# Kernel optimization log

Measured on AMD Instinct MI355X. Metric: run time of the kernel, lower is better.

## Reference

```python
import math
import jax, jax.numpy as jnp
import numpy as np

B, H, S, D = 2, 16, 2048, 64

def setup_inputs() -> dict:
    key = jax.random.key(0)
    kq, kk, kv = jax.random.split(key, 3)
    return {
        "query": jax.random.normal(kq, (B, H, S, D), dtype=jnp.float32),
        "key": jax.random.normal(kk, (B, H, S, D), dtype=jnp.float32),
        "value": jax.random.normal(kv, (B, H, S, D), dtype=jnp.float32),
        "mask": jnp.ones((B, S, 1), dtype=jnp.float32),  # padding mask, 1 = keep
        "mask_now": 0,  # 0 -> causal (tril diag=0); 1 -> strict causal (diag=-1)
    }

def reference(query, key, value, mask, mask_now):
    d_k = query.shape[-1]
    seq_len = mask.shape[1]
    # [B,H,S,S] scaled scores
    attn_scores = jnp.einsum("bhqd,bhkd->bhqk", query, key) / math.sqrt(d_k)
    diag = -1 if mask_now else 0
    triu_mask = jnp.tril(jnp.ones((seq_len, seq_len), dtype=mask.dtype), diag)  # [S,S]
    # mask[:, :, 0] -> per-query padding mask broadcast over key dim: [B,1,S,S]
    full_mask = triu_mask[None, None, :, :] * mask[:, None, :, 0:1]
    attn_scores = jnp.where(full_mask == 0, jnp.float32(-1e9), attn_scores)
    attn_scores = jax.nn.softmax(attn_scores, axis=-1)
    output = jnp.einsum("bhqk,bhkd->bhqd", attn_scores, value)
    return (output, attn_scores)
```

## Files before the change

### kernel.cpp

```cpp
#include <hip/hip_runtime.h>
#include <math.h>

#define NB 2
#define NH 16
#define SL 2048
#define DD 64
#define KC 64
#define NCH (SL / KC)
#define NT 256
#define LPS 68

typedef short bf16x8 __attribute__((ext_vector_type(8)));
typedef float f32x4  __attribute__((ext_vector_type(4)));

__device__ __forceinline__ unsigned short f2bf(float x) {
    unsigned u = __float_as_uint(x);
    u += 0x7fffu + ((u >> 16) & 1u);
    return (unsigned short)(u >> 16);
}

__device__ __forceinline__ void lds_barrier() {
    asm volatile("s_waitcnt lgkmcnt(0)\n\ts_barrier" ::: "memory");
}

__global__ __launch_bounds__(256)
void cvt_bf16(const float* __restrict__ in, unsigned short* __restrict__ out,
              int n4, float scale)
{
    int i = blockIdx.x * 256 + threadIdx.x;
    if (i >= n4) return;
    float4 v = ((const float4*)in)[i];
    ushort4 o;
    o.x = f2bf(v.x * scale); o.y = f2bf(v.y * scale);
    o.z = f2bf(v.z * scale); o.w = f2bf(v.w * scale);
    ((ushort4*)out)[i] = o;
}

__global__ __launch_bounds__(256)
void transpose_v(const float* __restrict__ V, unsigned short* __restrict__ Vt)
{
    __shared__ __align__(16) unsigned short vt[64 * 72];
    const int bh = blockIdx.x >> 5;
    const int s0 = (blockIdx.x & 31) * 64;
    const int t  = threadIdx.x;

    const float4* src = (const float4*)(V + ((size_t)bh * SL + s0) * DD);
    #pragma unroll
    for (int i = 0; i < 4; ++i) {
        int idx = t + i * 256;
        int r = idx >> 4, d4 = idx & 15;
        float4 v = src[r * 16 + d4];
        vt[(d4 * 4 + 0) * 72 + r] = f2bf(v.x);
        vt[(d4 * 4 + 1) * 72 + r] = f2bf(v.y);
        vt[(d4 * 4 + 2) * 72 + r] = f2bf(v.z);
        vt[(d4 * 4 + 3) * 72 + r] = f2bf(v.w);
    }
    __syncthreads();
    const int d = t >> 2, seg = t & 3;
    unsigned short* dst = Vt + ((size_t)bh * DD + d) * SL + s0 + seg * 16;
    uint4 p0 = *(const uint4*)&vt[d * 72 + seg * 16];
    uint4 p1 = *(const uint4*)&vt[d * 72 + seg * 16 + 8];
    *(uint4*)dst = p0;
    *(uint4*)(dst + 8) = p1;
}

__global__ __launch_bounds__(NT, 4)
void attn_mfma(const unsigned short* __restrict__ Qb,
               const unsigned short* __restrict__ Kb,
               const unsigned short* __restrict__ Vt,
               const float* __restrict__ Mg,
               const int* __restrict__ MNg,
               float* __restrict__ Og)
{
    __shared__ __align__(16) float ps[4][16 * LPS];
    __shared__ float lsx[4][16];

    const int tid  = threadIdx.x;
    const int w    = tid >> 6;
    const int lane = tid & 63;
    const int l15  = lane & 15;
    const int qd   = lane >> 4;

    const int lin  = blockIdx.x;
    const int xcd  = lin & 7;
    const int iloc = lin >> 3;
    const int bh   = xcd * 4 + (iloc >> 6);
    const int g    = iloc & 63;
    const int j    = (iloc >> 5) & 7;
    const int b    = bh >> 4;

    const int role  = (w + j) & 3;
    const int khalf = role & 1;
    const int r0    = (role < 2) ? g * 16 : 2032 - g * 16;

    const int diag = (MNg[0] != 0) ? -1 : 0;

    int rlim[4]; int anyDeg = 0;
    #pragma unroll
    for (int reg = 0; reg < 4; ++reg) {
        int row = r0 + qd * 4 + reg;
        float m = Mg[(size_t)b * SL + row];
        int rl = row + diag;
        if (m == 0.0f) rl = -1;
        rlim[reg] = rl;
        anyDeg |= (rl < 0);
    }
    const bool grpDeg = __any(anyDeg);
    const int lastB = grpDeg ? (NCH - 1) : ((r0 + 15 + diag) >> 6);
    const int N     = lastB + 1;
    const int kcMid = N >> 1;
    const int kcBeg = khalf ? kcMid : 0;
    const int kcEnd = khalf ? N : kcMid;

    const unsigned short* Qh  = Qb + (size_t)bh * SL * DD;
    const unsigned short* Kh  = Kb + (size_t)bh * SL * DD;
    const unsigned short* Vth = Vt + (size_t)bh * DD * SL;
    float* Oo   = Og + ((size_t)bh * SL + r0) * DD;
    float* Sout = Og + (size_t)NB * NH * SL * DD
                     + (size_t)bh * SL * SL + (size_t)r0 * SL;
    float* slab = ps[role];

    const unsigned short* qrow = Qh + (size_t)(r0 + l15) * DD + qd * 8;
    bf16x8 qf0 = *(const bf16x8*)qrow;
    bf16x8 qf1 = *(const bf16x8*)(qrow + 32);

    auto ldK = [&](int it, bf16x8& f0, bf16x8& f1) {
        const unsigned short* kr = Kh + (size_t)(it * 16 + l15) * DD + qd * 8;
        f0 = *(const bf16x8*)kr;
        f1 = *(const bf16x8*)(kr + 32);
    };

    float lacc[4] = {0.0f, 0.0f, 0.0f, 0.0f};
    {
        const int t0 = kcBeg * 4;
        const int T  = (kcEnd - kcBeg) * 4;
        auto cmpA = [&](int it, bf16x8 f0, bf16x8 f1) {
            f32x4 acc = {0.0f, 0.0f, 0.0f, 0.0f};
            __builtin_amdgcn_s_setprio(1);
            acc = __builtin_amdgcn_mfma_f32_16x16x32_bf16(qf0, f0, acc, 0, 0, 0);
            acc = __builtin_amdgcn_mfma_f32_16x16x32_bf16(qf1, f1, acc, 0, 0, 0);
            __builtin_amdgcn_s_setprio(0);
            const int col = it * 16 + l15;
            #pragma unroll
            for (int reg = 0; reg < 4; ++reg)
                lacc[reg] += (col <= rlim[reg]) ? __builtin_exp2f(acc[reg]) : 0.0f;
        };
        if (T > 0) {
            bf16x8 A0, A1, B0, B1;
            ldK(t0, A0, A1);
            for (int t = 0; t < T; t += 2) {
                if (t + 1 < T) ldK(t0 + t + 1, B0, B1);
                cmpA(t0 + t, A0, A1);
                if (t + 2 < T) ldK(t0 + t + 2, A0, A1);
                if (t + 1 < T) cmpA(t0 + t + 1, B0, B1);
            }
        }
    }

    float lsum[4];
    #pragma unroll
    for (int reg = 0; reg < 4; ++reg) {
        float s = lacc[reg];
        s += __shfl_xor(s, 1);  s += __shfl_xor(s, 2);
        s += __shfl_xor(s, 4);  s += __shfl_xor(s, 8);
        lsum[reg] = s;
    }
    if (l15 == 0) {
        #pragma unroll
        for (int reg = 0; reg < 4; ++reg)
            lsx[role][qd * 4 + reg] = lsum[reg];
    }
    lds_barrier();
    float pmul[4], pfill[4];
    #pragma unroll
    for (int reg = 0; reg < 4; ++reg) {
        float tot = lsum[reg] + lsx[role ^ 1][qd * 4 + reg];
        pmul[reg]  = (rlim[reg] < 0) ? 0.0f : 1.0f / tot;
        pfill[reg] = (rlim[reg] < 0) ? (1.0f / (float)SL) : 0.0f;
    }

    f32x4 oacc[4];
    #pragma unroll
    for (int nt = 0; nt < 4; ++nt) oacc[nt] = (f32x4){0.0f, 0.0f, 0.0f, 0.0f};

    for (int kc = kcBeg; kc < kcEnd; ++kc) {
        const int c0 = kc * KC;
        bf16x8 kb0[2], kb1[2];
        ldK(kc * 4, kb0[0], kb1[0]);
        #pragma unroll
        for (int nt = 0; nt < 4; ++nt) {
            if (nt < 3) ldK(kc * 4 + nt + 1, kb0[(nt + 1) & 1], kb1[(nt + 1) & 1]);
            f32x4 acc = {0.0f, 0.0f, 0.0f, 0.0f};
            __builtin_amdgcn_s_setprio(1);
            acc = __builtin_amdgcn_mfma_f32_16x16x32_bf16(qf0, kb0[nt & 1], acc, 0, 0, 0);
            acc = __builtin_amdgcn_mfma_f32_16x16x32_bf16(qf1, kb1[nt & 1], acc, 0, 0, 0);
            __builtin_amdgcn_s_setprio(0);
            const int col = c0 + nt * 16 + l15;
            #pragma unroll
            for (int reg = 0; reg < 4; ++reg) {
                float val = (col <= rlim[reg]) ? __builtin_exp2f(acc[reg]) * pmul[reg]
                                               : pfill[reg];
                slab[(qd * 4 + reg) * LPS + nt * 16 + l15] = val;
            }
        }
        bf16x8 vb0[2], vb1[2];
        {
            const unsigned short* vr = Vth + (size_t)l15 * SL + c0 + qd * 8;
            vb0[0] = *(const bf16x8*)vr;
            vb1[0] = *(const bf16x8*)(vr + 32);
        }
        #pragma unroll
        for (int ii = 0; ii < 4; ++ii) {
            int idx = ii * 64 + lane;
            int rr = idx >> 4, c4 = idx & 15;
            *(float4*)(Sout + (size_t)rr * SL + c0 + c4 * 4) =
                *(const float4*)&slab[rr * LPS + c4 * 4];
        }
        bf16x8 paf[2];
        #pragma unroll
        for (int kb = 0; kb < 2; ++kb) {
            const float* pr = &slab[l15 * LPS + kb * 32 + qd * 8];
            float4 x = *(const float4*)pr;
            float4 y = *(const float4*)(pr + 4);
            bf16x8 f;
            f[0] = (short)f2bf(x.x); f[1] = (short)f2bf(x.y);
            f[2] = (short)f2bf(x.z); f[3] = (short)f2bf(x.w);
            f[4] = (short)f2bf(y.x); f[5] = (short)f2bf(y.y);
            f[6] = (short)f2bf(y.z); f[7] = (short)f2bf(y.w);
            paf[kb] = f;
        }
        #pragma unroll
        for (int nt = 0; nt < 4; ++nt) {
            if (nt < 3) {
                const unsigned short* vr = Vth + (size_t)((nt + 1) * 16 + l15) * SL + c0 + qd * 8;
                vb0[(nt + 1) & 1] = *(const bf16x8*)vr;
                vb1[(nt + 1) & 1] = *(const bf16x8*)(vr + 32);
            }
            __builtin_amdgcn_s_setprio(1);
            oacc[nt] = __builtin_amdgcn_mfma_f32_16x16x32_bf16(paf[0], vb0[nt & 1], oacc[nt], 0, 0, 0);
            oacc[nt] = __builtin_amdgcn_mfma_f32_16x16x32_bf16(paf[1], vb1[nt & 1], oacc[nt], 0, 0, 0);
            __builtin_amdgcn_s_setprio(0);
        }
    }

    {
        const int zMid = N + ((NCH - N) >> 1);
        const int zb = khalf ? zMid : N;
        const int ze = khalf ? NCH : zMid;
        float4 z = make_float4(0.0f, 0.0f, 0.0f, 0.0f);
        for (int kc = zb; kc < ze; ++kc) {
            const int c0 = kc * KC;
            #pragma unroll
            for (int ii = 0; ii < 4; ++ii) {
                int idx = ii * 64 + lane;
                int rr = idx >> 4, c4 = idx & 15;
                *(float4*)(Sout + (size_t)rr * SL + c0 + c4 * 4) = z;
            }
        }
    }

    #pragma unroll
    for (int nt = 0; nt < 4; ++nt)
        #pragma unroll
        for (int reg = 0; reg < 4; ++reg)
            slab[(qd * 4 + reg) * LPS + nt * 16 + l15] = oacc[nt][reg];
    lds_barrier();
    {
        const float* sA = ps[role & ~1];
        const float* sB = ps[role | 1];
        #pragma unroll
        for (int ii = 0; ii < 2; ++ii) {
            int idx = ii * 64 + lane;
            int rr = (idx >> 4) + khalf * 8;
            int c4 = idx & 15;
            float4 a = *(const float4*)&sA[rr * LPS + c4 * 4];
            float4 bv = *(const float4*)&sB[rr * LPS + c4 * 4];
            float4 o = make_float4(a.x + bv.x, a.y + bv.y, a.z + bv.z, a.w + bv.w);
            *(float4*)(Oo + (size_t)rr * DD + c4 * 4) = o;
        }
    }
}

extern "C" void kernel_launch(void* const* d_in, const int* in_sizes, int n_in,
                              void* d_out, int out_size, void* d_ws, size_t ws_size,
                              hipStream_t stream)
{
    const float* q  = (const float*)d_in[0];
    const float* k  = (const float*)d_in[1];
    const float* v  = (const float*)d_in[2];
    const float* mk = (const float*)d_in[3];
    const int*   mn = (const int*)d_in[4];
    float* out = (float*)d_out;

    const size_t nElem = (size_t)NB * NH * SL * DD;
    unsigned short* Qb = (unsigned short*)d_ws;
    unsigned short* Kp = Qb + nElem;
    unsigned short* Vp = Kp + nElem;

    const int n4 = (int)(nElem / 4);
    cvt_bf16<<<n4 / 256, 256, 0, stream>>>(q, Qb, n4, 0.125f * 1.44269504f);
    cvt_bf16<<<n4 / 256, 256, 0, stream>>>(k, Kp, n4, 1.0f);
    transpose_v<<<NB * NH * (SL / 64), 256, 0, stream>>>(v, Vp);

    attn_mfma<<<2048, NT, 0, stream>>>(Qb, Kp, Vp, mk, mn, out);
}
```

Baseline: 744.5 us.

## Raise occupancy target and drop software-pipelined K/V register prefetch

Raises the launch-bounds minimum blocks per CU from 4 to 8, which forces the compiler to use fewer registers. To fit that budget it removes the double-buffered K and V fragment prefetching in the normalization pass and the main loop, loading each fragment right before its MFMA. It also rewrites the zero-fill of masked score columns so each half-wave fills 8 full rows contiguously instead of splitting chunks. The intent is to hide latency through more resident waves rather than explicit prefetch, at the risk of exposed load latency per wave and possible register spills.

```diff
diff --git a/kernel.cpp b/kernel.cpp
--- a/kernel.cpp
+++ b/kernel.cpp
@@ -64,7 +64,7 @@
     *(uint4*)(dst + 8) = p1;
 }
 
-__global__ __launch_bounds__(NT, 4)
+__global__ __launch_bounds__(NT, 8)
 void attn_mfma(const unsigned short* __restrict__ Qb,
                const unsigned short* __restrict__ Kb,
                const unsigned short* __restrict__ Vt,
@@ -124,37 +124,20 @@
     bf16x8 qf0 = *(const bf16x8*)qrow;
     bf16x8 qf1 = *(const bf16x8*)(qrow + 32);
 
-    auto ldK = [&](int it, bf16x8& f0, bf16x8& f1) {
+    float lacc[4] = {0.0f, 0.0f, 0.0f, 0.0f};
+    for (int it = kcBeg * 4; it < kcEnd * 4; ++it) {
         const unsigned short* kr = Kh + (size_t)(it * 16 + l15) * DD + qd * 8;
-        f0 = *(const bf16x8*)kr;
-        f1 = *(const bf16x8*)(kr + 32);
-    };
-
-    float lacc[4] = {0.0f, 0.0f, 0.0f, 0.0f};
-    {
-        const int t0 = kcBeg * 4;
-        const int T  = (kcEnd - kcBeg) * 4;
-        auto cmpA = [&](int it, bf16x8 f0, bf16x8 f1) {
-            f32x4 acc = {0.0f, 0.0f, 0.0f, 0.0f};
-            __builtin_amdgcn_s_setprio(1);
-            acc = __builtin_amdgcn_mfma_f32_16x16x32_bf16(qf0, f0, acc, 0, 0, 0);
-            acc = __builtin_amdgcn_mfma_f32_16x16x32_bf16(qf1, f1, acc, 0, 0, 0);
-            __builtin_amdgcn_s_setprio(0);
-            const int col = it * 16 + l15;
-            #pragma unroll
-            for (int reg = 0; reg < 4; ++reg)
-                lacc[reg] += (col <= rlim[reg]) ? __builtin_exp2f(acc[reg]) : 0.0f;
-        };
-        if (T > 0) {
-            bf16x8 A0, A1, B0, B1;
-            ldK(t0, A0, A1);
-            for (int t = 0; t < T; t += 2) {
-                if (t + 1 < T) ldK(t0 + t + 1, B0, B1);
-                cmpA(t0 + t, A0, A1);
-                if (t + 2 < T) ldK(t0 + t + 2, A0, A1);
-                if (t + 1 < T) cmpA(t0 + t + 1, B0, B1);
-            }
-        }
+        bf16x8 f0 = *(const bf16x8*)kr;
+        bf16x8 f1 = *(const bf16x8*)(kr + 32);
+        f32x4 acc = {0.0f, 0.0f, 0.0f, 0.0f};
+        __builtin_amdgcn_s_setprio(1);
+        acc = __builtin_amdgcn_mfma_f32_16x16x32_bf16(qf0, f0, acc, 0, 0, 0);
+        acc = __builtin_amdgcn_mfma_f32_16x16x32_bf16(qf1, f1, acc, 0, 0, 0);
+        __builtin_amdgcn_s_setprio(0);
+        const int col = it * 16 + l15;
+        #pragma unroll
+        for (int reg = 0; reg < 4; ++reg)
+            lacc[reg] += (col <= rlim[reg]) ? __builtin_exp2f(acc[reg]) : 0.0f;
     }
 
     float lsum[4];
@@ -185,15 +168,15 @@
 
     for (int kc = kcBeg; kc < kcEnd; ++kc) {
         const int c0 = kc * KC;
-        bf16x8 kb0[2], kb1[2];
-        ldK(kc * 4, kb0[0], kb1[0]);
         #pragma unroll
         for (int nt = 0; nt < 4; ++nt) {
-            if (nt < 3) ldK(kc * 4 + nt + 1, kb0[(nt + 1) & 1], kb1[(nt + 1) & 1]);
+            const unsigned short* kr = Kh + (size_t)(c0 + nt * 16 + l15) * DD + qd * 8;
+            bf16x8 f0 = *(const bf16x8*)kr;
+            bf16x8 f1 = *(const bf16x8*)(kr + 32);
             f32x4 acc = {0.0f, 0.0f, 0.0f, 0.0f};
             __builtin_amdgcn_s_setprio(1);
-            acc = __builtin_amdgcn_mfma_f32_16x16x32_bf16(qf0, kb0[nt & 1], acc, 0, 0, 0);
-            acc = __builtin_amdgcn_mfma_f32_16x16x32_bf16(qf1, kb1[nt & 1], acc, 0, 0, 0);
+            acc = __builtin_amdgcn_mfma_f32_16x16x32_bf16(qf0, f0, acc, 0, 0, 0);
+            acc = __builtin_amdgcn_mfma_f32_16x16x32_bf16(qf1, f1, acc, 0, 0, 0);
             __builtin_amdgcn_s_setprio(0);
             const int col = c0 + nt * 16 + l15;
             #pragma unroll
@@ -202,12 +185,6 @@
                                                : pfill[reg];
                 slab[(qd * 4 + reg) * LPS + nt * 16 + l15] = val;
             }
-        }
-        bf16x8 vb0[2], vb1[2];
-        {
-            const unsigned short* vr = Vth + (size_t)l15 * SL + c0 + qd * 8;
-            vb0[0] = *(const bf16x8*)vr;
-            vb1[0] = *(const bf16x8*)(vr + 32);
         }
         #pragma unroll
         for (int ii = 0; ii < 4; ++ii) {
@@ -231,31 +208,24 @@
         }
         #pragma unroll
         for (int nt = 0; nt < 4; ++nt) {
-            if (nt < 3) {
-                const unsigned short* vr = Vth + (size_t)((nt + 1) * 16 + l15) * SL + c0 + qd * 8;
-                vb0[(nt + 1) & 1] = *(const bf16x8*)vr;
-                vb1[(nt + 1) & 1] = *(const bf16x8*)(vr + 32);
-            }
+            const unsigned short* vr = Vth + (size_t)(nt * 16 + l15) * SL + c0 + qd * 8;
+            bf16x8 v0 = *(const bf16x8*)vr;
+            bf16x8 v1 = *(const bf16x8*)(vr + 32);
             __builtin_amdgcn_s_setprio(1);
-            oacc[nt] = __builtin_amdgcn_mfma_f32_16x16x32_bf16(paf[0], vb0[nt & 1], oacc[nt], 0, 0, 0);
-            oacc[nt] = __builtin_amdgcn_mfma_f32_16x16x32_bf16(paf[1], vb1[nt & 1], oacc[nt], 0, 0, 0);
+            oacc[nt] = __builtin_amdgcn_mfma_f32_16x16x32_bf16(paf[0], v0, oacc[nt], 0, 0, 0);
+            oacc[nt] = __builtin_amdgcn_mfma_f32_16x16x32_bf16(paf[1], v1, oacc[nt], 0, 0, 0);
             __builtin_amdgcn_s_setprio(0);
         }
     }
 
     {
-        const int zMid = N + ((NCH - N) >> 1);
-        const int zb = khalf ? zMid : N;
-        const int ze = khalf ? NCH : zMid;
+        const int zc0 = N * KC;
+        const int rbeg = khalf * 8;
         float4 z = make_float4(0.0f, 0.0f, 0.0f, 0.0f);
-        for (int kc = zb; kc < ze; ++kc) {
-            const int c0 = kc * KC;
-            #pragma unroll
-            for (int ii = 0; ii < 4; ++ii) {
-                int idx = ii * 64 + lane;
-                int rr = idx >> 4, c4 = idx & 15;
-                *(float4*)(Sout + (size_t)rr * SL + c0 + c4 * 4) = z;
-            }
+        for (int rr = rbeg; rr < rbeg + 8; ++rr) {
+            float* rowp = Sout + (size_t)rr * SL;
+            for (int c = zc0 + (lane << 2); c < SL; c += 256)
+                *(float4*)(rowp + c) = z;
         }
     }
 
```

Measured after the change: 802.0 us. 7.7% more time.
